# Optimization experiments

Hardware: AMD Instinct MI355X
Metric: run time of the kernel (lower is better)

The kernel has to match this reference:

```python
import jax, jax.numpy as jnp
import numpy as np

B, S, DIM, E, K = 8, 8192, 512, 4, 2
EPS = 1e-6


def setup_inputs() -> dict:
    key = jax.random.key(0)
    ks = jax.random.split(key, 4)
    scale = 0.02
    return {
        "x": jax.random.normal(ks[0], (B, S, DIM), dtype=jnp.float32),
        "router_w": jax.random.normal(ks[1], (DIM, E), dtype=jnp.float32) * scale,
        "router_b": jnp.zeros((E,), jnp.float32),
        "expert_w": jax.random.normal(ks[2], (E, DIM, DIM), dtype=jnp.float32) * scale,
        "expert_b": jnp.zeros((E, DIM), jnp.float32),
        "out_w": jax.random.normal(ks[3], (DIM, DIM), dtype=jnp.float32) * scale,
        "out_b": jnp.zeros((DIM,), jnp.float32),
        "norm_w": jnp.ones((DIM,), jnp.float32),
    }


def reference(x, router_w, router_b, expert_w, expert_b, out_w, out_b, norm_w):
    b, s, d = x.shape
    # router
    logits = x @ router_w + router_b                      # [B,S,E]
    topw, topi = jax.lax.top_k(logits, K)                 # [B,S,K]
    topw = jax.nn.softmax(topw, axis=-1)
    t = b * s
    xf = x.reshape(t, d)
    idx = topi.reshape(t, K)
    w = topw.reshape(t, K).astype(x.dtype)
    # dense token-expert weight mask (topk indices are distinct per token)
    mask = jnp.zeros((t, E), x.dtype).at[jnp.arange(t)[:, None], idx].set(w)
    # expert FFN: Linear + SiLU (dropout disabled in eval)
    h = jax.nn.silu(jnp.einsum("td,edh->teh", xf, expert_w) + expert_b)  # [T,E,D]
    comb = jnp.einsum("te,teh->th", mask, h)              # weighted combine
    out = comb @ out_w + out_b
    y = xf + out                                          # residual
    rms = jnp.sqrt(jnp.mean(y * y, axis=-1, keepdims=True) + EPS)
    return (norm_w * (y / rms)).reshape(b, s, d)
```

## Files before the change

kernel.cpp:

```cpp
#include <hip/hip_runtime.h>
#include <hip/hip_bf16.h>
#include <stdint.h>

#define NTOK 65536
#define DIM 512
#define NEXP 4
#define REG 14336

using u16 = unsigned short;
using u32 = unsigned int;
typedef __attribute__((ext_vector_type(4))) float f32x4;
typedef __attribute__((ext_vector_type(8))) short bf16x8;
typedef __attribute__((ext_vector_type(8))) u16 u16x8;
typedef __attribute__((ext_vector_type(4))) u16 u16x4;

__device__ __forceinline__ u16 f2bf(float f) {
  u32 u = __builtin_bit_cast(u32, f);
  u32 r = (u + 0x7FFFu + ((u >> 16) & 1u)) >> 16;
  return (u16)r;
}
__device__ __forceinline__ float bf2f(u16 v) {
  return __builtin_bit_cast(float, (u32)v << 16);
}

#define GLOAD_LDS16(gp, lp)                                                    \
  __builtin_amdgcn_global_load_lds(                                            \
      (const __attribute__((address_space(1))) void*)(gp),                     \
      (__attribute__((address_space(3))) void*)(lp), 16, 0, 0)

#define FENCE asm volatile("" ::: "memory")
#define BARRIER { FENCE; __builtin_amdgcn_s_barrier(); FENCE; }
#define LGKM0 { asm volatile("s_waitcnt lgkmcnt(0)" ::: "memory"); __builtin_amdgcn_sched_barrier(0); }
#define VMCNT_(n) asm volatile("s_waitcnt vmcnt(" #n ")" ::: "memory")
#define VMCNT(n) VMCNT_(n)

__device__ __forceinline__ const bf16x8* lds_frag(const u16* base, int row, int chunk) {
  return (const bf16x8*)((const char*)base + row * 128 + (((chunk) ^ (row & 7)) << 4));
}
__device__ __forceinline__ const bf16x8* frag32(const u16* base, int row, int rchByte) {
  return (const bf16x8*)((const char*)base + row * 64 + rchByte);
}

__global__ void wconv(const float* __restrict__ ew, u16* __restrict__ ewt,
                      int* __restrict__ cnt) {
  __shared__ float tile[32][33];
  int mat = blockIdx.y;
  if (blockIdx.x == 0 && mat == 0 && threadIdx.x < 6) cnt[threadIdx.x] = 0;
  const float* s = ew + (size_t)mat * DIM * DIM;
  u16* d = ewt + (size_t)mat * DIM * DIM;
  int tx = blockIdx.x & 15, ty = blockIdx.x >> 4;
  int lx = threadIdx.x & 31, ly0 = threadIdx.x >> 5;
#pragma unroll
  for (int i = 0; i < 4; ++i) {
    int ly = ly0 + i * 8;
    tile[ly][lx] = s[(size_t)(ty * 32 + ly) * DIM + tx * 32 + lx];
  }
  __syncthreads();
#pragma unroll
  for (int i = 0; i < 4; ++i) {
    int ly = ly0 + i * 8;
    d[(size_t)(tx * 32 + ly) * DIM + ty * 32 + lx] = f2bf(tile[lx][ly]);
  }
}

__global__ void owpack(const float* __restrict__ ow, u16* __restrict__ owt3) {
  int lane = threadIdx.x & 63, wv = threadIdx.x >> 6;
  int frag = blockIdx.x * 4 + wv;
  int j = frag & 7, kc = (frag >> 3) & 1, t = (frag >> 4) & 7, strip = frag >> 7;
  int r16 = lane & 15, lg = lane >> 4;
  int h = strip * 128 + j * 16 + r16;
  int d0 = t * 64 + kc * 32 + lg * 8;
  u16x8 o;
#pragma unroll
  for (int q = 0; q < 8; ++q) o[q] = f2bf(ow[(size_t)(d0 + q) * DIM + h]);
  *(u16x8*)(owt3 + (size_t)frag * 512 + lane * 8) = o;
}

__global__ void router_kernel(const float* __restrict__ x, const float* __restrict__ rw,
                              const float* __restrict__ rb, u16* __restrict__ xb,
                              int* __restrict__ pp, float2* __restrict__ wab) {
  int lane = threadIdx.x & 63, wave = threadIdx.x >> 6;
  size_t t = (size_t)blockIdx.x * 4 + wave;
  const float* xr = x + t * DIM + lane * 8;
  f32x4 v0 = *(const f32x4*)xr;
  f32x4 v1 = *(const f32x4*)(xr + 4);
  float l0 = 0.f, l1 = 0.f, l2 = 0.f, l3 = 0.f;
  const float* rwp = rw + (size_t)lane * 32;
#pragma unroll
  for (int j = 0; j < 8; ++j) {
    float xv = (j < 4) ? v0[j] : v1[j - 4];
    f32x4 r = *(const f32x4*)(rwp + j * 4);
    l0 += xv * r[0]; l1 += xv * r[1]; l2 += xv * r[2]; l3 += xv * r[3];
  }
#pragma unroll
  for (int off = 32; off; off >>= 1) {
    l0 += __shfl_xor(l0, off); l1 += __shfl_xor(l1, off);
    l2 += __shfl_xor(l2, off); l3 += __shfl_xor(l3, off);
  }
  float lv[4] = {l0 + rb[0], l1 + rb[1], l2 + rb[2], l3 + rb[3]};
  int i0 = 0; float b0 = lv[0];
#pragma unroll
  for (int e = 1; e < 4; ++e) if (lv[e] > b0) { b0 = lv[e]; i0 = e; }
  int i1 = (i0 == 0) ? 1 : 0; float b1 = lv[i1];
#pragma unroll
  for (int e = 0; e < 4; ++e) if (e != i0 && lv[e] > b1) { b1 = lv[e]; i1 = e; }
  float ex = __expf(b1 - b0);
  float w0 = 1.0f / (1.0f + ex);
  float w1 = ex * w0;
  if (lane == 0) {
    int a = (i0 < i1) ? i0 : i1;
    int b = (i0 < i1) ? i1 : i0;
    const int ptab[16] = {-1, 0, 1, 2, -1, -1, 3, 4, -1, -1, -1, 5, -1, -1, -1, -1};
    pp[t] = ptab[a * 4 + b];
    float wa = (a == i0) ? w0 : w1;
    float wb = (a == i0) ? w1 : w0;
    wab[t] = make_float2(wa, wb);
  }
  u16x8 o;
#pragma unroll
  for (int j = 0; j < 4; ++j) { o[j] = f2bf(v0[j]); o[4 + j] = f2bf(v1[j]); }
  *(u16x8*)(xb + t * DIM + lane * 8) = o;
}

__global__ void assignscatter(const int* __restrict__ pp, const float2* __restrict__ wab,
                              int* __restrict__ cnt, int* __restrict__ list,
                              float2* __restrict__ wpair) {
  int t = blockIdx.x * 256 + threadIdx.x;
  int lane = threadIdx.x & 63;
  int p = pp[t];
  float2 w = wab[t];
  int pos = 0;
#pragma unroll
  for (int q = 0; q < 6; ++q) {
    unsigned long long m = __ballot(p == q);
    if (p == q) {
      int rank = __popcll(m & ((1ull << lane) - 1ull));
      int leader = __ffsll((long long)m) - 1;
      int base = 0;
      if (lane == leader) base = atomicAdd(&cnt[q], (int)__popcll(m));
      base = __shfl(base, leader);
      pos = base + rank;
    }
  }
  int slot = p * REG + pos;
  if (pos < REG) {
    list[slot] = t;
    wpair[slot] = w;
  }
}

__global__ __launch_bounds__(256, 2) void expert_gemm(
    const u16* __restrict__ xb, const u16* __restrict__ ewt,
    const float* __restrict__ ebias, const int* __restrict__ cnt,
    const int* __restrict__ list, const float2* __restrict__ wpair,
    u16* __restrict__ comb) {
  __shared__ u16 Asl[3][128 * 32];
  __shared__ u16 Bal[3][128 * 32];
  __shared__ u16 Bbl[3][128 * 32];
  int tid = threadIdx.x, lane = tid & 63, wave = tid >> 6;
  int wy = wave >> 1, wx = wave & 1;
  int b = blockIdx.x;
  int chunk = b >> 5, within = b & 31;
  int panel = chunk * 8 + (within & 7);
  int nblk = within >> 3;
  int p = panel / (REG / 128);
  int m0 = panel * 128;
  int cntp = cnt[p];
  if (m0 - p * REG >= cntp) return;
  int n0 = nblk * 128;
  const int ea2[6] = {0, 0, 0, 1, 1, 2};
  const int eb2[6] = {1, 2, 3, 2, 3, 3};
  int eA = ea2[p], eB = eb2[p];

  int r4 = lane >> 2, c4 = lane & 3;
  int rot = (r4 >> 1) & 3;
  int kch = ((c4 - rot) & 3) * 8;
  int r16 = lane & 15, lg = lane >> 4;
  int rchB = (((lg + ((r16 >> 1) & 3)) & 3)) * 16;

  int sid2[2];
#pragma unroll
  for (int j = 0; j < 2; ++j) {
    int slot = m0 + wave * 32 + j * 16 + r4;
    int idv = list[slot];
    sid2[j] = ((slot - p * REG) < cntp) ? idv : 0;
  }
  const u16* a0b = xb + (size_t)sid2[0] * DIM + kch;
  const u16* a1b = xb + (size_t)sid2[1] * DIM + kch;
  const u16* bab = ewt + (size_t)eA * DIM * DIM + (size_t)(n0 + wave * 32 + r4) * DIM + kch;
  const u16* bbb = ewt + (size_t)eB * DIM * DIM + (size_t)(n0 + wave * 32 + r4) * DIM + kch;

  f32x4 accA[4][4], accB[4][4];
#pragma unroll
  for (int i = 0; i < 4; ++i)
#pragma unroll
    for (int j = 0; j < 4; ++j) { accA[i][j] = (f32x4)(0.f); accB[i][j] = (f32x4)(0.f); }

#define STAGE(BI, KS)                                                          \
  do {                                                                         \
    GLOAD_LDS16(a0b + (KS) * 32, Asl[BI] + (wave * 32) * 32);                  \
    GLOAD_LDS16(a1b + (KS) * 32, Asl[BI] + (wave * 32 + 16) * 32);             \
    GLOAD_LDS16(bab + (KS) * 32, Bal[BI] + (wave * 32) * 32);                  \
    GLOAD_LDS16(bab + 16 * DIM + (KS) * 32, Bal[BI] + (wave * 32 + 16) * 32);  \
    GLOAD_LDS16(bbb + (KS) * 32, Bbl[BI] + (wave * 32) * 32);                  \
    GLOAD_LDS16(bbb + 16 * DIM + (KS) * 32, Bbl[BI] + (wave * 32 + 16) * 32);  \
  } while (0)

  STAGE(0, 0); STAGE(1, 1);
  VMCNT(6);
  BARRIER;

#define KST(T, WC)                                                             \
  {                                                                            \
    if ((T) + 2 < 16) STAGE(((T) + 2) % 3, (T) + 2);                           \
    bf16x8 a[4], ba[4], bb[4];                                                 \
    _Pragma("unroll") for (int i = 0; i < 4; ++i) {                            \
      a[i]  = *frag32(Asl[(T) % 3], wy * 64 + i * 16 + r16, rchB);             \
      ba[i] = *frag32(Bal[(T) % 3], wx * 64 + i * 16 + r16, rchB);             \
      bb[i] = *frag32(Bbl[(T) % 3], wx * 64 + i * 16 + r16, rchB);             \
    }                                                                          \
    __builtin_amdgcn_s_setprio(1);                                             \
    _Pragma("unroll") for (int i = 0; i < 4; ++i)                              \
      _Pragma("unroll") for (int j = 0; j < 4; ++j)                            \
        accA[i][j] = __builtin_amdgcn_mfma_f32_16x16x32_bf16(a[i], ba[j], accA[i][j], 0, 0, 0); \
    _Pragma("unroll") for (int i = 0; i < 4; ++i)                              \
      _Pragma("unroll") for (int j = 0; j < 4; ++j)                            \
        accB[i][j] = __builtin_amdgcn_mfma_f32_16x16x32_bf16(a[i], bb[j], accB[i][j], 0, 0, 0); \
    __builtin_amdgcn_s_setprio(0);                                             \
    WC;                                                                        \
  }

  KST(0,  { VMCNT(6); BARRIER; })
  KST(1,  { VMCNT(6); BARRIER; })
  KST(2,  { VMCNT(6); BARRIER; })
  KST(3,  { VMCNT(6); BARRIER; })
  KST(4,  { VMCNT(6); BARRIER; })
  KST(5,  { VMCNT(6); BARRIER; })
  KST(6,  { VMCNT(6); BARRIER; })
  KST(7,  { VMCNT(6); BARRIER; })
  KST(8,  { VMCNT(6); BARRIER; })
  KST(9,  { VMCNT(6); BARRIER; })
  KST(10, { VMCNT(6); BARRIER; })
  KST(11, { VMCNT(6); BARRIER; })
  KST(12, { VMCNT(6); BARRIER; })
  KST(13, { VMCNT(6); BARRIER; })
  KST(14, { VMCNT(0); BARRIER; })
  KST(15, {})
#undef KST
#undef STAGE

  float bA4[4], bB4[4];
#pragma unroll
  for (int j = 0; j < 4; ++j) {
    int h = n0 + wx * 64 + j * 16 + r16;
    bA4[j] = ebias[eA * DIM + h];
    bB4[j] = ebias[eB * DIM + h];
  }
#pragma unroll
  for (int i = 0; i < 4; ++i) {
    int rb = wy * 64 + i * 16 + lg * 4;
#pragma unroll
    for (int rr = 0; rr < 4; ++rr) {
      int slot = m0 + rb + rr;
      bool val = (slot - p * REG) < cntp;
      int id = list[slot];
      float2 wv = wpair[slot];
#pragma unroll
      for (int j = 0; j < 4; ++j) {
        float zA = accA[i][j][rr] + bA4[j];
        float zB = accB[i][j][rr] + bB4[j];
        float sA = zA / (1.0f + __expf(-zA));
        float sB = zB / (1.0f + __expf(-zB));
        float v = wv.x * sA + wv.y * sB;
        if (val) {
          int h = n0 + wx * 64 + j * 16 + r16;
          comb[(size_t)id * DIM + h] = f2bf(v);
        }
      }
    }
  }
}

__global__ __launch_bounds__(256, 2) void outnorm(
    const u16* __restrict__ comb, const u16* __restrict__ owt3,
    const float* __restrict__ ob, const u16* __restrict__ xb,
    const float* __restrict__ nw, float* __restrict__ out) {
  __shared__ u16 As[3][64 * 64];
  __shared__ float rowsum[64][4];
  int tid = threadIdx.x, lane = tid & 63, w = tid >> 6;
  int m0 = blockIdx.x * 64;
  int r16 = lane & 15, lg = lane >> 4;
  int rl = lane >> 3;
  int scb = ((lane & 7) ^ rl) * 8;
  int n0w = w * 128;

  f32x4 acc[8][4];
#pragma unroll
  for (int j = 0; j < 8; ++j)
#pragma unroll
    for (int i = 0; i < 4; ++i) acc[j][i] = (f32x4)(0.f);

#define OSTG(bi, ks)                                                           \
  _Pragma("unroll") for (int jj = 0; jj < 2; ++jj) {                           \
    GLOAD_LDS16(comb + (size_t)(m0 + w * 16 + jj * 8 + rl) * DIM + (ks) * 64 + scb, \
                As[bi] + (w * 16 + jj * 8) * 64);                              \
  }
#define LOADB(BV, HH)                                                          \
  {                                                                            \
    const u16* bp_ = owt3 +                                                    \
        ((size_t)(((w * 8 + ((HH) >> 1)) * 2 + ((HH) & 1)) * 8)) * 512 + lane * 8; \
    _Pragma("unroll") for (int jj = 0; jj < 8; ++jj)                           \
      BV[jj] = *(const bf16x8*)(bp_ + jj * 512);                               \
  }
#define HSTEP(H, BC, BN, WC)                                                   \
  {                                                                            \
    if (((H) & 1) == 0 && ((H) >> 1) + 2 < 8) OSTG((((H) >> 1) + 2) % 3, ((H) >> 1) + 2); \
    if ((H) + 1 < 16) LOADB(BN, (H) + 1);                                      \
    bf16x8 af[4];                                                              \
    _Pragma("unroll") for (int ii = 0; ii < 4; ++ii)                           \
      af[ii] = *lds_frag(As[((H) >> 1) % 3], ii * 16 + r16, ((H) & 1) * 4 + lg); \
    LGKM0;                                                                     \
    __builtin_amdgcn_s_setprio(1);                                             \
    _Pragma("unroll") for (int jj = 0; jj < 8; ++jj)                           \
      _Pragma("unroll") for (int ii = 0; ii < 4; ++ii)                         \
        acc[jj][ii] = __builtin_amdgcn_mfma_f32_16x16x32_bf16(BC[jj], af[ii], acc[jj][ii], 0, 0, 0); \
    __builtin_amdgcn_s_setprio(0);                                             \
    WC;                                                                        \
  }

  bf16x8 BE[8], BO[8];
  OSTG(0, 0); OSTG(1, 1);
  LOADB(BE, 0);
  VMCNT(10);
  BARRIER;

  HSTEP(0,  BE, BO, {})
  HSTEP(1,  BO, BE, { VMCNT(10); BARRIER; })
  HSTEP(2,  BE, BO, {})
  HSTEP(3,  BO, BE, { VMCNT(10); BARRIER; })
  HSTEP(4,  BE, BO, {})
  HSTEP(5,  BO, BE, { VMCNT(10); BARRIER; })
  HSTEP(6,  BE, BO, {})
  HSTEP(7,  BO, BE, { VMCNT(10); BARRIER; })
  HSTEP(8,  BE, BO, {})
  HSTEP(9,  BO, BE, { VMCNT(10); BARRIER; })
  HSTEP(10, BE, BO, {})
  HSTEP(11, BO, BE, { VMCNT(10); BARRIER; })
  HSTEP(12, BE, BO, {})
  HSTEP(13, BO, BE, { VMCNT(8); BARRIER; })
  HSTEP(14, BE, BO, {})
  HSTEP(15, BO, BE, {})
#undef HSTEP
#undef LOADB
#undef OSTG

  float part[4] = {0.f, 0.f, 0.f, 0.f};
#pragma unroll
  for (int hj = 0; hj < 8; ++hj) {
    int h0 = n0w + hj * 16 + lg * 4;
    f32x4 obv = *(const f32x4*)(ob + h0);
#pragma unroll
    for (int ti = 0; ti < 4; ++ti) {
      int t = m0 + ti * 16 + r16;
      u16x4 xv4 = *(const u16x4*)(xb + (size_t)t * DIM + h0);
#pragma unroll
      for (int rr = 0; rr < 4; ++rr) {
        float yv = bf2f(xv4[rr]) + acc[hj][ti][rr] + obv[rr];
        acc[hj][ti][rr] = yv;
        part[ti] += yv * yv;
      }
    }
  }
#pragma unroll
  for (int ti = 0; ti < 4; ++ti) {
    part[ti] += __shfl_xor(part[ti], 16);
    part[ti] += __shfl_xor(part[ti], 32);
  }
  if (lane < 16) {
#pragma unroll
    for (int ti = 0; ti < 4; ++ti) rowsum[ti * 16 + r16][w] = part[ti];
  }
  __syncthreads();
  float inv[4];
#pragma unroll
  for (int ti = 0; ti < 4; ++ti) {
    int tr = ti * 16 + r16;
    float s = rowsum[tr][0] + rowsum[tr][1] + rowsum[tr][2] + rowsum[tr][3];
    inv[ti] = 1.0f / sqrtf(s * (1.0f / 512.0f) + 1e-6f);
  }
#pragma unroll
  for (int hj = 0; hj < 8; ++hj) {
    int h0 = n0w + hj * 16 + lg * 4;
    f32x4 nwv = *(const f32x4*)(nw + h0);
#pragma unroll
    for (int ti = 0; ti < 4; ++ti) {
      int t = m0 + ti * 16 + r16;
      f32x4 o;
#pragma unroll
      for (int rr = 0; rr < 4; ++rr) o[rr] = acc[hj][ti][rr] * inv[ti] * nwv[rr];
      *(f32x4*)(out + (size_t)t * DIM + h0) = o;
    }
  }
}

extern "C" void kernel_launch(void* const* d_in, const int* in_sizes, int n_in,
                              void* d_out, int out_size, void* d_ws, size_t ws_size,
                              hipStream_t stream) {
  const float* x  = (const float*)d_in[0];
  const float* rw = (const float*)d_in[1];
  const float* rb = (const float*)d_in[2];
  const float* ew = (const float*)d_in[3];
  const float* eb = (const float*)d_in[4];
  const float* ow = (const float*)d_in[5];
  const float* ob = (const float*)d_in[6];
  const float* nw = (const float*)d_in[7];
  float* out = (float*)d_out;

  char* ws = (char*)d_ws;
  u16*   xb    = (u16*)(ws);
  u16*   combb = (u16*)(ws + 67108864);
  int*   pp    = (int*)(ws + 67108864);
  float2* wab  = (float2*)(ws + 67108864 + 262144);
  u16*   ewt   = (u16*)(ws + 134217728);
  u16*   owt3  = (u16*)(ws + 136314880);
  int*   list  = (int*)(ws + 136839168);
  float2* wpair = (float2*)(ws + 136839168 + 344064);
  int*   cnt   = (int*)(ws + 136839168 + 344064 + 688128);

  wconv<<<dim3(256, 4), 256, 0, stream>>>(ew, ewt, cnt);
  owpack<<<128, 256, 0, stream>>>(ow, owt3);
  router_kernel<<<NTOK / 4, 256, 0, stream>>>(x, rw, rb, xb, pp, wab);
  assignscatter<<<NTOK / 256, 256, 0, stream>>>(pp, wab, cnt, list, wpair);
  expert_gemm<<<dim3(6 * REG / 128 * 4), 256, 0, stream>>>(xb, ewt, eb, cnt, list, wpair, combb);
  outnorm<<<dim3(NTOK / 64), 256, 0, stream>>>(combb, owt3, ob, xb, nw, out);
}
```

Before: 329.7 us.

## Prepack expert weights into MFMA fragment layout and load B directly to registers

Replaces the expert-weight transpose kernel with a pack kernel that writes bf16 weights already in per-lane MFMA fragment order. The expert GEMM then loads B fragments straight from global memory into double-buffered registers, which removes the two B LDS buffers and their LDS reads. Only the token tile A still goes through LDS. This cuts LDS traffic and footprint, but raises register pressure and makes each wave fetch its own B from global/L2 instead of sharing it through LDS.

```diff
diff --git a/kernel.cpp b/kernel.cpp
--- a/kernel.cpp
+++ b/kernel.cpp
@@ -33,6 +33,7 @@
 #define LGKM0 { asm volatile("s_waitcnt lgkmcnt(0)" ::: "memory"); __builtin_amdgcn_sched_barrier(0); }
 #define VMCNT_(n) asm volatile("s_waitcnt vmcnt(" #n ")" ::: "memory")
 #define VMCNT(n) VMCNT_(n)
+#define SB __builtin_amdgcn_sched_barrier(0)
 
 __device__ __forceinline__ const bf16x8* lds_frag(const u16* base, int row, int chunk) {
   return (const bf16x8*)((const char*)base + row * 128 + (((chunk) ^ (row & 7)) << 4));
@@ -41,26 +42,20 @@
   return (const bf16x8*)((const char*)base + row * 64 + rchByte);
 }
 
-__global__ void wconv(const float* __restrict__ ew, u16* __restrict__ ewt,
-                      int* __restrict__ cnt) {
-  __shared__ float tile[32][33];
-  int mat = blockIdx.y;
-  if (blockIdx.x == 0 && mat == 0 && threadIdx.x < 6) cnt[threadIdx.x] = 0;
-  const float* s = ew + (size_t)mat * DIM * DIM;
-  u16* d = ewt + (size_t)mat * DIM * DIM;
-  int tx = blockIdx.x & 15, ty = blockIdx.x >> 4;
-  int lx = threadIdx.x & 31, ly0 = threadIdx.x >> 5;
-#pragma unroll
-  for (int i = 0; i < 4; ++i) {
-    int ly = ly0 + i * 8;
-    tile[ly][lx] = s[(size_t)(ty * 32 + ly) * DIM + tx * 32 + lx];
-  }
-  __syncthreads();
-#pragma unroll
-  for (int i = 0; i < 4; ++i) {
-    int ly = ly0 + i * 8;
-    d[(size_t)(tx * 32 + ly) * DIM + ty * 32 + lx] = f2bf(tile[lx][ly]);
-  }
+__global__ void ewpack(const float* __restrict__ ew, u16* __restrict__ ewtp,
+                       int* __restrict__ cnt) {
+  if (blockIdx.x == 0 && threadIdx.x < 6) cnt[threadIdx.x] = 0;
+  int lane = threadIdx.x & 63, wv = threadIdx.x >> 6;
+  int f = blockIdx.x * 4 + wv;
+  int hs = f & 31, T = (f >> 5) & 15, e = f >> 9;
+  int r16 = lane & 15, lg = lane >> 4;
+  int h = hs * 16 + r16;
+  int d0 = T * 32 + lg * 8;
+  u16x8 o;
+#pragma unroll
+  for (int q = 0; q < 8; ++q)
+    o[q] = f2bf(ew[((size_t)e * DIM + d0 + q) * DIM + h]);
+  *(u16x8*)(ewtp + (size_t)f * 512 + lane * 8) = o;
 }
 
 __global__ void owpack(const float* __restrict__ ow, u16* __restrict__ owt3) {
@@ -150,13 +145,11 @@
 }
 
 __global__ __launch_bounds__(256, 2) void expert_gemm(
-    const u16* __restrict__ xb, const u16* __restrict__ ewt,
+    const u16* __restrict__ xb, const u16* __restrict__ ewtp,
     const float* __restrict__ ebias, const int* __restrict__ cnt,
     const int* __restrict__ list, const float2* __restrict__ wpair,
     u16* __restrict__ comb) {
   __shared__ u16 Asl[3][128 * 32];
-  __shared__ u16 Bal[3][128 * 32];
-  __shared__ u16 Bbl[3][128 * 32];
   int tid = threadIdx.x, lane = tid & 63, wave = tid >> 6;
   int wy = wave >> 1, wx = wave & 1;
   int b = blockIdx.x;
@@ -187,8 +180,8 @@
   }
   const u16* a0b = xb + (size_t)sid2[0] * DIM + kch;
   const u16* a1b = xb + (size_t)sid2[1] * DIM + kch;
-  const u16* bab = ewt + (size_t)eA * DIM * DIM + (size_t)(n0 + wave * 32 + r4) * DIM + kch;
-  const u16* bbb = ewt + (size_t)eB * DIM * DIM + (size_t)(n0 + wave * 32 + r4) * DIM + kch;
+  const u16* bpA = ewtp + (size_t)eA * 262144 + (size_t)(n0 / 16 + wx * 4) * 512 + lane * 8;
+  const u16* bpB = ewtp + (size_t)eB * 262144 + (size_t)(n0 / 16 + wx * 4) * 512 + lane * 8;
 
   f32x4 accA[4][4], accB[4][4];
 #pragma unroll
@@ -200,53 +193,60 @@
   do {                                                                         \
     GLOAD_LDS16(a0b + (KS) * 32, Asl[BI] + (wave * 32) * 32);                  \
     GLOAD_LDS16(a1b + (KS) * 32, Asl[BI] + (wave * 32 + 16) * 32);             \
-    GLOAD_LDS16(bab + (KS) * 32, Bal[BI] + (wave * 32) * 32);                  \
-    GLOAD_LDS16(bab + 16 * DIM + (KS) * 32, Bal[BI] + (wave * 32 + 16) * 32);  \
-    GLOAD_LDS16(bbb + (KS) * 32, Bbl[BI] + (wave * 32) * 32);                  \
-    GLOAD_LDS16(bbb + 16 * DIM + (KS) * 32, Bbl[BI] + (wave * 32 + 16) * 32);  \
   } while (0)
-
-  STAGE(0, 0); STAGE(1, 1);
-  VMCNT(6);
+#define LOADBX(BV, S)                                                          \
+  do {                                                                         \
+    _Pragma("unroll") for (int i = 0; i < 4; ++i) {                            \
+      BV[i]     = *(const bf16x8*)(bpA + (S) * 16384 + i * 512);               \
+      BV[4 + i] = *(const bf16x8*)(bpB + (S) * 16384 + i * 512);               \
+    }                                                                          \
+  } while (0)
+
+  bf16x8 BE[8], BO[8];
+  STAGE(0, 0); SB;
+  STAGE(1, 1); SB;
+  LOADBX(BE, 0); SB;
+  VMCNT(10);
   BARRIER;
 
-#define KST(T, WC)                                                             \
+#define KST(T, BC, BN, WC)                                                     \
   {                                                                            \
-    if ((T) + 2 < 16) STAGE(((T) + 2) % 3, (T) + 2);                           \
-    bf16x8 a[4], ba[4], bb[4];                                                 \
-    _Pragma("unroll") for (int i = 0; i < 4; ++i) {                            \
-      a[i]  = *frag32(Asl[(T) % 3], wy * 64 + i * 16 + r16, rchB);             \
-      ba[i] = *frag32(Bal[(T) % 3], wx * 64 + i * 16 + r16, rchB);             \
-      bb[i] = *frag32(Bbl[(T) % 3], wx * 64 + i * 16 + r16, rchB);             \
-    }                                                                          \
+    if ((T) + 1 < 16) { LOADBX(BN, (T) + 1); }                                 \
+    SB;                                                                        \
+    if ((T) + 2 < 16) { STAGE(((T) + 2) % 3, (T) + 2); }                       \
+    SB;                                                                        \
+    bf16x8 a[4];                                                               \
+    _Pragma("unroll") for (int i = 0; i < 4; ++i)                              \
+      a[i] = *frag32(Asl[(T) % 3], wy * 64 + i * 16 + r16, rchB);              \
     __builtin_amdgcn_s_setprio(1);                                             \
     _Pragma("unroll") for (int i = 0; i < 4; ++i)                              \
       _Pragma("unroll") for (int j = 0; j < 4; ++j)                            \
-        accA[i][j] = __builtin_amdgcn_mfma_f32_16x16x32_bf16(a[i], ba[j], accA[i][j], 0, 0, 0); \
+        accA[i][j] = __builtin_amdgcn_mfma_f32_16x16x32_bf16(a[i], BC[j], accA[i][j], 0, 0, 0); \
     _Pragma("unroll") for (int i = 0; i < 4; ++i)                              \
       _Pragma("unroll") for (int j = 0; j < 4; ++j)                            \
-        accB[i][j] = __builtin_amdgcn_mfma_f32_16x16x32_bf16(a[i], bb[j], accB[i][j], 0, 0, 0); \
+        accB[i][j] = __builtin_amdgcn_mfma_f32_16x16x32_bf16(a[i], BC[4 + j], accB[i][j], 0, 0, 0); \
     __builtin_amdgcn_s_setprio(0);                                             \
     WC;                                                                        \
   }
 
-  KST(0,  { VMCNT(6); BARRIER; })
-  KST(1,  { VMCNT(6); BARRIER; })
-  KST(2,  { VMCNT(6); BARRIER; })
-  KST(3,  { VMCNT(6); BARRIER; })
-  KST(4,  { VMCNT(6); BARRIER; })
-  KST(5,  { VMCNT(6); BARRIER; })
-  KST(6,  { VMCNT(6); BARRIER; })
-  KST(7,  { VMCNT(6); BARRIER; })
-  KST(8,  { VMCNT(6); BARRIER; })
-  KST(9,  { VMCNT(6); BARRIER; })
-  KST(10, { VMCNT(6); BARRIER; })
-  KST(11, { VMCNT(6); BARRIER; })
-  KST(12, { VMCNT(6); BARRIER; })
-  KST(13, { VMCNT(6); BARRIER; })
-  KST(14, { VMCNT(0); BARRIER; })
-  KST(15, {})
+  KST(0,  BE, BO, { VMCNT(2); BARRIER; })
+  KST(1,  BO, BE, { VMCNT(2); BARRIER; })
+  KST(2,  BE, BO, { VMCNT(2); BARRIER; })
+  KST(3,  BO, BE, { VMCNT(2); BARRIER; })
+  KST(4,  BE, BO, { VMCNT(2); BARRIER; })
+  KST(5,  BO, BE, { VMCNT(2); BARRIER; })
+  KST(6,  BE, BO, { VMCNT(2); BARRIER; })
+  KST(7,  BO, BE, { VMCNT(2); BARRIER; })
+  KST(8,  BE, BO, { VMCNT(2); BARRIER; })
+  KST(9,  BO, BE, { VMCNT(2); BARRIER; })
+  KST(10, BE, BO, { VMCNT(2); BARRIER; })
+  KST(11, BO, BE, { VMCNT(2); BARRIER; })
+  KST(12, BE, BO, { VMCNT(2); BARRIER; })
+  KST(13, BO, BE, { VMCNT(2); BARRIER; })
+  KST(14, BE, BO, { VMCNT(2); BARRIER; })
+  KST(15, BO, BE, {})
 #undef KST
+#undef LOADBX
 #undef STAGE
 
   float bA4[4], bB4[4];
@@ -421,16 +421,16 @@
   u16*   combb = (u16*)(ws + 67108864);
   int*   pp    = (int*)(ws + 67108864);
   float2* wab  = (float2*)(ws + 67108864 + 262144);
-  u16*   ewt   = (u16*)(ws + 134217728);
+  u16*   ewtp  = (u16*)(ws + 134217728);
   u16*   owt3  = (u16*)(ws + 136314880);
   int*   list  = (int*)(ws + 136839168);
   float2* wpair = (float2*)(ws + 136839168 + 344064);
   int*   cnt   = (int*)(ws + 136839168 + 344064 + 688128);
 
-  wconv<<<dim3(256, 4), 256, 0, stream>>>(ew, ewt, cnt);
+  ewpack<<<512, 256, 0, stream>>>(ew, ewtp, cnt);
   owpack<<<128, 256, 0, stream>>>(ow, owt3);
   router_kernel<<<NTOK / 4, 256, 0, stream>>>(x, rw, rb, xb, pp, wab);
   assignscatter<<<NTOK / 256, 256, 0, stream>>>(pp, wab, cnt, list, wpair);
-  expert_gemm<<<dim3(6 * REG / 128 * 4), 256, 0, stream>>>(xb, ewt, eb, cnt, list, wpair, combb);
+  expert_gemm<<<dim3(6 * REG / 128 * 4), 256, 0, stream>>>(xb, ewtp, eb, cnt, list, wpair, combb);
   outnorm<<<dim3(NTOK / 64), 256, 0, stream>>>(combb, owt3, ob, xb, nw, out);
 }
```

Measured after the change: 321.7 us. 1.02x faster.
